# Kernel optimization log

Measured on AMD Instinct MI355X. Metric: run time of the kernel, lower is better.

Reference implementation:

```python
import jax, jax.numpy as jnp
import numpy as np
from jax import lax

Q = 8          # num quantization bins (co_matrix_shape[0])
K = 3          # spatial filter size (spatial_shape = [K,K,K])
PAD = (K - 1) // 2


def setup_inputs() -> dict:
    key = jax.random.key(0)
    k1, k2, k3 = jax.random.split(key, 3)
    # uniform [0,1) so floor((x-min)/max * Q) stays in [0, Q-1] (matches valid torch index_select)
    x = jax.random.uniform(k1, (8, 16, 256, 256), dtype=jnp.float32)
    co_matrix = jax.random.normal(k2, (Q, Q), dtype=jnp.float32)
    spatial_filter = jax.random.normal(k3, (K, K, K), dtype=jnp.float32)
    return {"input": x, "co_matrix": co_matrix, "spatial_filter": spatial_filter}


def _quantize(x, num_q):
    # faithful to the torch code: norm = (x - min) / max  (NOT max-min)
    x_min = jnp.min(x)
    x_max = jnp.max(x)
    idx = jnp.floor((x - x_min) / x_max * num_q).astype(jnp.int32)  # [N,c,h,w]
    return idx


def reference(input, co_matrix, spatial_filter):
    x = input
    N, c, h, w = x.shape
    idx = _quantize(x, Q)                                  # [N,c,h,w] int32

    # Vectorize the per-bin loop: gather row i of co_matrix at every pixel's bin index.
    # cof[i] = co_matrix[i, idx]  -> [Q,N,c,h,w]
    cof = co_matrix[:, idx]
    conv_in = (cof * x[None]).reshape(Q * N, 1, c, h, w)   # [Q*N,1,c,h,w]

    w3d = spatial_filter.reshape(1, 1, K, K, K)
    spatial = lax.conv_general_dilated(
        conv_in, w3d,
        window_strides=(1, 1, 1),
        padding=[(PAD, PAD)] * 3,
        dimension_numbers=("NCDHW", "OIDHW", "NCDHW"),
    ).reshape(Q, N, c, h, w)

    # torch code convolves the mask with a 1x1x1 ones filter at stride 1 -> identity
    mask = (idx[None] == jnp.arange(Q, dtype=jnp.int32)[:, None, None, None, None])
    conv_out = jnp.sum(mask.astype(x.dtype) * spatial, axis=0)  # [N,c,h,w]
    return (conv_out, co_matrix, spatial_filter, idx)
```

## Files before the change

### kernel.cpp

```cpp
#include <hip/hip_runtime.h>
#include <stdint.h>

#define LISTBASE 4096
#define QCAP     4096

__global__ __launch_bounds__(256) void k_minmax(const float* __restrict__ x, int n4, int ntail,
                                                float* __restrict__ partials) {
  __shared__ float smn[256], smx[256];
  int tid = threadIdx.x;
  float mn = 3.0e38f, mx = -3.0e38f;
  const float4* x4 = (const float4*)x;
  for (int i = blockIdx.x * blockDim.x + tid; i < n4; i += gridDim.x * blockDim.x) {
    float4 v = x4[i];
    mn = fminf(mn, fminf(fminf(v.x, v.y), fminf(v.z, v.w)));
    mx = fmaxf(mx, fmaxf(fmaxf(v.x, v.y), fmaxf(v.z, v.w)));
  }
  if (blockIdx.x == 0 && tid == 0) {
    for (int i = 4 * n4; i < 4 * n4 + ntail; ++i) { mn = fminf(mn, x[i]); mx = fmaxf(mx, x[i]); }
  }
  smn[tid] = mn; smx[tid] = mx;
  __syncthreads();
  for (int s = 128; s > 0; s >>= 1) {
    if (tid < s) { smn[tid] = fminf(smn[tid], smn[tid + s]); smx[tid] = fmaxf(smx[tid], smx[tid + s]); }
    __syncthreads();
  }
  if (tid == 0) { partials[2 * blockIdx.x] = smn[0]; partials[2 * blockIdx.x + 1] = smx[0]; }
}

__global__ __launch_bounds__(256) void k_params(const float* __restrict__ partials, int nb,
                                                const float* __restrict__ co, const float* __restrict__ sfil,
                                                float* __restrict__ ws,
                                                float* __restrict__ out_co, float* __restrict__ out_sf) {
  __shared__ float smn[256], smx[256];
  int tid = threadIdx.x;
  float mn = 3.0e38f, mx = -3.0e38f;
  for (int i = tid; i < nb; i += 256) { mn = fminf(mn, partials[2 * i]); mx = fmaxf(mx, partials[2 * i + 1]); }
  smn[tid] = mn; smx[tid] = mx;
  __syncthreads();
  for (int s = 128; s > 0; s >>= 1) {
    if (tid < s) { smn[tid] = fminf(smn[tid], smn[tid + s]); smx[tid] = fmaxf(smx[tid], smx[tid + s]); }
    __syncthreads();
  }
  if (tid == 0) {
    ws[0] = smn[0]; ws[1] = smx[0];
    ws[2] = 1.0f / smx[0];
    ((uint32_t*)ws)[3] = 0u;
  }
  if (tid < 8) {
    const float* r = co + tid * 8;
    float rmn = r[0], rmx = r[0];
    #pragma unroll
    for (int j = 1; j < 8; ++j) { rmn = fminf(rmn, r[j]); rmx = fmaxf(rmx, r[j]); }
    float rs = (rmx - rmn) * (1.0f / 255.0f);
    if (rs < 1e-30f) rs = 1.0f;
    uint32_t d0 = 0, d1 = 0;
    #pragma unroll
    for (int j = 0; j < 8; ++j) {
      int b = (int)lrintf((r[j] - rmn) / rs);
      b = b < 0 ? 0 : (b > 255 ? 255 : b);
      if (j < 4) d0 |= ((uint32_t)b) << (8 * j);
      else       d1 |= ((uint32_t)b) << (8 * (j - 4));
    }
    uint32_t* wsu = (uint32_t*)ws;
    wsu[8 + 4 * tid + 0] = d0;
    wsu[8 + 4 * tid + 1] = d1;
    wsu[8 + 4 * tid + 2] = __float_as_uint(rs);
    wsu[8 + 4 * tid + 3] = __float_as_uint(rmn);
  }
  if (tid < 64) out_co[tid] = co[tid];
  if (tid < 27) out_sf[tid] = sfil[tid];
}

__global__ __launch_bounds__(256) void k_conv(const float* __restrict__ x, const float* __restrict__ sfil,
                                              float* __restrict__ ws, int listcap,
                                              float* __restrict__ out, float* __restrict__ out_idx) {
  __shared__ __align__(16) float    xs[7920];
  __shared__ __align__(16) uint32_t qls[1980];
  __shared__ __align__(16) uint4    tbl[8];

  int tid = threadIdx.x;
  int b = blockIdx.x;
  int wt = b & 1, ht = (b >> 1) & 31, ct = (b >> 6) & 3, n = b >> 8;
  int c0 = ct * 4, h0 = ht * 8, w0 = wt * 128;
  int nbase = n * 16;

  const uint32_t* wsu = (const uint32_t*)ws;
  if (tid < 8) tbl[tid] = ((const uint4*)(wsu + 8))[tid];

  float mn = ws[0], mx = ws[1], y = ws[2];
  uint32_t* cnt = (uint32_t*)ws + 3;
  int* list = (int*)ws + LISTBASE;

  for (int e = tid; e < 1980; e += 256) {
    int lc = e / 330;
    int r  = e - lc * 330;
    int lh = r / 33;
    int lg = r - lh * 33;
    int c = c0 - 1 + lc, h = h0 - 1 + lh, wb = w0 - 1 + 4 * lg;
    bool chok = ((unsigned)c < 16u) & ((unsigned)h < 256u);
    int gofs = ((nbase + c) << 16) + (h << 8) + wb;
    float xv[4]; int qi[4]; uint32_t qu[4];
    #pragma unroll
    for (int j = 0; j < 4; ++j) {
      float xj = 0.0f;
      if (chok & ((unsigned)(wb + j) < 256u)) xj = x[gofs + j];
      float s  = xj - mn;
      float t0 = s * y;
      float r0 = __builtin_fmaf(-mx, t0, s);
      float t1 = __builtin_fmaf(r0, y, t0);
      float r1 = __builtin_fmaf(-mx, t1, s);
      float d  = __builtin_fmaf(r1, y, t1);
      int q = (int)(d * 8.0f);
      xv[j] = xj; qi[j] = q;
      qu[j] = (uint32_t)(q > 7 ? 7 : q);
    }
    if (((qi[0] | qi[1] | qi[2] | qi[3]) & 8) != 0) {
      #pragma unroll
      for (int j = 0; j < 4; ++j) if (qi[j] == 8) {
        uint32_t slot = atomicAdd(cnt, 1u);
        if (slot < (uint32_t)listcap) list[slot] = gofs + j;
      }
    }
    uint32_t b01 = __builtin_amdgcn_perm(qu[1], qu[0], 0x0c0c0400u);
    uint32_t b23 = __builtin_amdgcn_perm(qu[3], qu[2], 0x04000c0cu);
    int ro = lc * 10 + lh;
    *(float4*)&xs[ro * 132 + 4 * lg] = float4{xv[0], xv[1], xv[2], xv[3]};
    qls[ro * 33 + lg] = b01 | b23;
  }
  __syncthreads();

  float wf[27];
  #pragma unroll
  for (int i = 0; i < 27; ++i) wf[i] = sfil[i];

  const int tw = tid & 31, th = tid >> 5;
  const uint32_t SELK[4] = {0x03020100u, 0x04030201u, 0x05040302u, 0x06050403u};

  for (int c = 0; c < 4; ++c) {
    int xbase = (c * 10 + th) * 132 + 4 * tw;
    int qbase = (c * 10 + th) * 33 + tw;

    int qc = qbase + 11 * 33;
    uint32_t Qc0 = qls[qc], Qc1 = qls[qc + 1];
    uint32_t q4 = __builtin_amdgcn_perm(Qc1, Qc0, 0x04030201u);
    uint32_t rlo[4], rhi[4]; float rs4[4], rc4[4];
    #pragma unroll
    for (int k = 0; k < 4; ++k) {
      uint32_t qk = (q4 >> (8 * k)) & 0xffu;
      uint4 T = tbl[qk];
      rlo[k] = T.x; rhi[k] = T.y;
      rs4[k] = __uint_as_float(T.z); rc4[k] = __uint_as_float(T.w);
    }

    float acc1[4] = {0.f, 0.f, 0.f, 0.f};
    float acc2[4] = {0.f, 0.f, 0.f, 0.f};
    #pragma unroll
    for (int dc = 0; dc < 3; ++dc) {
      #pragma unroll
      for (int di = 0; di < 3; ++di) {
        int xo = xbase + (dc * 10 + di) * 132;
        float4 A = *(const float4*)&xs[xo];
        float2 B = *(const float2*)&xs[xo + 4];
        int qo = qbase + (dc * 10 + di) * 33;
        uint32_t Q0 = qls[qo], Q1 = qls[qo + 1];
        float xw[6] = {A.x, A.y, A.z, A.w, B.x, B.y};
        const float* wr = &wf[dc * 9 + di * 3];
        #pragma unroll
        for (int k = 0; k < 4; ++k) {
          uint32_t sel = __builtin_amdgcn_perm(Q1, Q0, SELK[k]);
          uint32_t bb  = __builtin_amdgcn_perm(rhi[k], rlo[k], sel);
          float b0 = (float)(bb & 0xffu);
          float b1 = (float)((bb >> 8) & 0xffu);
          float b2 = (float)((bb >> 16) & 0xffu);
          float p0 = wr[0] * xw[k];
          float p1 = wr[1] * xw[k + 1];
          float p2 = wr[2] * xw[k + 2];
          acc2[k] += p0 + p1 + p2;
          acc1[k] = __builtin_fmaf(p0, b0, acc1[k]);
          acc1[k] = __builtin_fmaf(p1, b1, acc1[k]);
          acc1[k] = __builtin_fmaf(p2, b2, acc1[k]);
        }
      }
    }
    int gbase = ((nbase + c0 + c) << 16) + ((h0 + th) << 8) + (w0 + 4 * tw);
    float4 o;
    o.x = __builtin_fmaf(rs4[0], acc1[0], rc4[0] * acc2[0]);
    o.y = __builtin_fmaf(rs4[1], acc1[1], rc4[1] * acc2[1]);
    o.z = __builtin_fmaf(rs4[2], acc1[2], rc4[2] * acc2[2]);
    o.w = __builtin_fmaf(rs4[3], acc1[3], rc4[3] * acc2[3]);
    *(float4*)&out[gbase] = o;
    out_idx[gbase + 0] = (float)(q4 & 0xffu);
    out_idx[gbase + 1] = (float)((q4 >> 8) & 0xffu);
    out_idx[gbase + 2] = (float)((q4 >> 16) & 0xffu);
    out_idx[gbase + 3] = (float)((q4 >> 24) & 0xffu);
  }
}

__global__ __launch_bounds__(256) void k_fix(const float* __restrict__ ws, int listcap,
                                             float* __restrict__ out, float* __restrict__ out_idx) {
  uint32_t n = ((const uint32_t*)ws)[3];
  if (n > (uint32_t)listcap) n = (uint32_t)listcap;
  const int* list = (const int*)ws + LISTBASE;
  for (uint32_t i = threadIdx.x; i < n; i += 256) {
    int p = list[i];
    out[p] = 0.0f;
    out_idx[p] = 8.0f;
  }
}

extern "C" void kernel_launch(void* const* d_in, const int* in_sizes, int n_in,
                              void* d_out, int out_size, void* d_ws, size_t ws_size,
                              hipStream_t stream) {
  const float* x    = (const float*)d_in[0];
  const float* co   = (const float*)d_in[1];
  const float* sfil = (const float*)d_in[2];
  float* out = (float*)d_out;
  float* ws  = (float*)d_ws;
  int nx = in_sizes[0];

  int nb1 = 1024;
  long wsd = (long)(ws_size / 4);
  long maxnb = (wsd - 64) / 2;
  if (maxnb > 2016) maxnb = 2016;
  if (nb1 > maxnb) nb1 = (int)(maxnb < 1 ? 1 : maxnb);
  int listcap = (int)(wsd - LISTBASE);
  if (listcap > QCAP) listcap = QCAP;
  if (listcap < 0) listcap = 0;

  float* partials = ws + 64;
  int n4 = nx / 4, ntail = nx - 4 * n4;

  float* out_co  = out + nx;
  float* out_sf  = out + nx + 64;
  float* out_idx = out + nx + 64 + 27;

  k_minmax<<<nb1, 256, 0, stream>>>(x, n4, ntail, partials);
  k_params<<<1, 256, 0, stream>>>(partials, nb1, co, sfil, ws, out_co, out_sf);
  k_conv<<<2048, 256, 0, stream>>>(x, sfil, ws, listcap, out, out_idx);
  k_fix<<<1, 256, 0, stream>>>(ws, listcap, out, out_idx);
}
```

Measured before the change: 139.9 us.

## Fuse min/max reduction via atomics, drop fix kernel, halve channel tile

Replaces the two-kernel min/max reduction with a single kernel that publishes its result through order-preserving atomicMin/atomicMax on mapped floats, with the co-matrix table setup folded into block 0. The separate fix-up kernel and its atomic overflow list are removed. The conv kernel now recomputes the exact quantization index for centre pixels, zeroing the output and writing index 8 in place. The conv tile shrinks from 4 channels to 2 and the grid doubles, which cuts shared memory per block at the cost of more halo reloads. Two memset calls are added to initialise the atomic slots.

Measured after the change: 182.5 us. +30.4%, slower.

```diff
diff --git a/kernel.cpp b/kernel.cpp
--- a/kernel.cpp
+++ b/kernel.cpp
@@ -1,11 +1,18 @@
 #include <hip/hip_runtime.h>
 #include <stdint.h>
 
-#define LISTBASE 4096
-#define QCAP     4096
+__device__ __forceinline__ uint32_t mapf(float f) {
+  uint32_t u = __float_as_uint(f);
+  return (u & 0x80000000u) ? ~u : (u | 0x80000000u);
+}
+__device__ __forceinline__ float unmapf(uint32_t m) {
+  return (m & 0x80000000u) ? __uint_as_float(m & 0x7FFFFFFFu) : __uint_as_float(~m);
+}
 
 __global__ __launch_bounds__(256) void k_minmax(const float* __restrict__ x, int n4, int ntail,
-                                                float* __restrict__ partials) {
+                                                const float* __restrict__ co, const float* __restrict__ sfil,
+                                                uint32_t* __restrict__ wsu,
+                                                float* __restrict__ out_co, float* __restrict__ out_sf) {
   __shared__ float smn[256], smx[256];
   int tid = threadIdx.x;
   float mn = 3.0e38f, mx = -3.0e38f;
@@ -24,74 +31,56 @@
     if (tid < s) { smn[tid] = fminf(smn[tid], smn[tid + s]); smx[tid] = fmaxf(smx[tid], smx[tid + s]); }
     __syncthreads();
   }
-  if (tid == 0) { partials[2 * blockIdx.x] = smn[0]; partials[2 * blockIdx.x + 1] = smx[0]; }
-}
-
-__global__ __launch_bounds__(256) void k_params(const float* __restrict__ partials, int nb,
-                                                const float* __restrict__ co, const float* __restrict__ sfil,
-                                                float* __restrict__ ws,
-                                                float* __restrict__ out_co, float* __restrict__ out_sf) {
-  __shared__ float smn[256], smx[256];
-  int tid = threadIdx.x;
-  float mn = 3.0e38f, mx = -3.0e38f;
-  for (int i = tid; i < nb; i += 256) { mn = fminf(mn, partials[2 * i]); mx = fmaxf(mx, partials[2 * i + 1]); }
-  smn[tid] = mn; smx[tid] = mx;
-  __syncthreads();
-  for (int s = 128; s > 0; s >>= 1) {
-    if (tid < s) { smn[tid] = fminf(smn[tid], smn[tid + s]); smx[tid] = fmaxf(smx[tid], smx[tid + s]); }
-    __syncthreads();
-  }
   if (tid == 0) {
-    ws[0] = smn[0]; ws[1] = smx[0];
-    ws[2] = 1.0f / smx[0];
-    ((uint32_t*)ws)[3] = 0u;
-  }
-  if (tid < 8) {
-    const float* r = co + tid * 8;
-    float rmn = r[0], rmx = r[0];
-    #pragma unroll
-    for (int j = 1; j < 8; ++j) { rmn = fminf(rmn, r[j]); rmx = fmaxf(rmx, r[j]); }
-    float rs = (rmx - rmn) * (1.0f / 255.0f);
-    if (rs < 1e-30f) rs = 1.0f;
-    uint32_t d0 = 0, d1 = 0;
-    #pragma unroll
-    for (int j = 0; j < 8; ++j) {
-      int b = (int)lrintf((r[j] - rmn) / rs);
-      b = b < 0 ? 0 : (b > 255 ? 255 : b);
-      if (j < 4) d0 |= ((uint32_t)b) << (8 * j);
-      else       d1 |= ((uint32_t)b) << (8 * (j - 4));
-    }
-    uint32_t* wsu = (uint32_t*)ws;
-    wsu[8 + 4 * tid + 0] = d0;
-    wsu[8 + 4 * tid + 1] = d1;
-    wsu[8 + 4 * tid + 2] = __float_as_uint(rs);
-    wsu[8 + 4 * tid + 3] = __float_as_uint(rmn);
-  }
-  if (tid < 64) out_co[tid] = co[tid];
-  if (tid < 27) out_sf[tid] = sfil[tid];
+    atomicMin(&wsu[0], mapf(smn[0]));
+    atomicMax(&wsu[1], mapf(smx[0]));
+  }
+  if (blockIdx.x == 0) {
+    if (tid < 8) {
+      const float* r = co + tid * 8;
+      float rmn = r[0], rmx = r[0];
+      #pragma unroll
+      for (int j = 1; j < 8; ++j) { rmn = fminf(rmn, r[j]); rmx = fmaxf(rmx, r[j]); }
+      float rs = (rmx - rmn) * (1.0f / 255.0f);
+      if (rs < 1e-30f) rs = 1.0f;
+      uint32_t d0 = 0, d1 = 0;
+      #pragma unroll
+      for (int j = 0; j < 8; ++j) {
+        int b = (int)lrintf((r[j] - rmn) / rs);
+        b = b < 0 ? 0 : (b > 255 ? 255 : b);
+        if (j < 4) d0 |= ((uint32_t)b) << (8 * j);
+        else       d1 |= ((uint32_t)b) << (8 * (j - 4));
+      }
+      wsu[8 + 4 * tid + 0] = d0;
+      wsu[8 + 4 * tid + 1] = d1;
+      wsu[8 + 4 * tid + 2] = __float_as_uint(rs);
+      wsu[8 + 4 * tid + 3] = __float_as_uint(rmn);
+    }
+    if (tid < 64) out_co[tid] = co[tid];
+    if (tid < 27) out_sf[tid] = sfil[tid];
+  }
 }
 
 __global__ __launch_bounds__(256) void k_conv(const float* __restrict__ x, const float* __restrict__ sfil,
-                                              float* __restrict__ ws, int listcap,
+                                              const uint32_t* __restrict__ wsu,
                                               float* __restrict__ out, float* __restrict__ out_idx) {
-  __shared__ __align__(16) float    xs[7920];
-  __shared__ __align__(16) uint32_t qls[1980];
+  __shared__ __align__(16) float    xs[5280];
+  __shared__ __align__(16) uint32_t qls[1320];
   __shared__ __align__(16) uint4    tbl[8];
 
   int tid = threadIdx.x;
   int b = blockIdx.x;
-  int wt = b & 1, ht = (b >> 1) & 31, ct = (b >> 6) & 3, n = b >> 8;
-  int c0 = ct * 4, h0 = ht * 8, w0 = wt * 128;
+  int wt = b & 1, ht = (b >> 1) & 31, ct = (b >> 6) & 7, n = b >> 9;
+  int c0 = ct * 2, h0 = ht * 8, w0 = wt * 128;
   int nbase = n * 16;
 
-  const uint32_t* wsu = (const uint32_t*)ws;
   if (tid < 8) tbl[tid] = ((const uint4*)(wsu + 8))[tid];
 
-  float mn = ws[0], mx = ws[1], y = ws[2];
-  uint32_t* cnt = (uint32_t*)ws + 3;
-  int* list = (int*)ws + LISTBASE;
-
-  for (int e = tid; e < 1980; e += 256) {
+  float mn = unmapf(wsu[0]);
+  float mx = unmapf(wsu[1]);
+  float y  = 1.0f / mx;
+
+  for (int e = tid; e < 1320; e += 256) {
     int lc = e / 330;
     int r  = e - lc * 330;
     int lh = r / 33;
@@ -99,7 +88,7 @@
     int c = c0 - 1 + lc, h = h0 - 1 + lh, wb = w0 - 1 + 4 * lg;
     bool chok = ((unsigned)c < 16u) & ((unsigned)h < 256u);
     int gofs = ((nbase + c) << 16) + (h << 8) + wb;
-    float xv[4]; int qi[4]; uint32_t qu[4];
+    float xv[4]; uint32_t qu[4];
     #pragma unroll
     for (int j = 0; j < 4; ++j) {
       float xj = 0.0f;
@@ -111,15 +100,8 @@
       float r1 = __builtin_fmaf(-mx, t1, s);
       float d  = __builtin_fmaf(r1, y, t1);
       int q = (int)(d * 8.0f);
-      xv[j] = xj; qi[j] = q;
+      xv[j] = xj;
       qu[j] = (uint32_t)(q > 7 ? 7 : q);
-    }
-    if (((qi[0] | qi[1] | qi[2] | qi[3]) & 8) != 0) {
-      #pragma unroll
-      for (int j = 0; j < 4; ++j) if (qi[j] == 8) {
-        uint32_t slot = atomicAdd(cnt, 1u);
-        if (slot < (uint32_t)listcap) list[slot] = gofs + j;
-      }
     }
     uint32_t b01 = __builtin_amdgcn_perm(qu[1], qu[0], 0x0c0c0400u);
     uint32_t b23 = __builtin_amdgcn_perm(qu[3], qu[2], 0x04000c0cu);
@@ -136,7 +118,7 @@
   const int tw = tid & 31, th = tid >> 5;
   const uint32_t SELK[4] = {0x03020100u, 0x04030201u, 0x05040302u, 0x06050403u};
 
-  for (int c = 0; c < 4; ++c) {
+  for (int c = 0; c < 2; ++c) {
     int xbase = (c * 10 + th) * 132 + 4 * tw;
     int qbase = (c * 10 + th) * 33 + tw;
 
@@ -154,6 +136,7 @@
 
     float acc1[4] = {0.f, 0.f, 0.f, 0.f};
     float acc2[4] = {0.f, 0.f, 0.f, 0.f};
+    float4 cxA; float2 cxB;
     #pragma unroll
     for (int dc = 0; dc < 3; ++dc) {
       #pragma unroll
@@ -161,6 +144,7 @@
         int xo = xbase + (dc * 10 + di) * 132;
         float4 A = *(const float4*)&xs[xo];
         float2 B = *(const float2*)&xs[xo + 4];
+        if (dc == 1 && di == 1) { cxA = A; cxB = B; }
         int qo = qbase + (dc * 10 + di) * 33;
         uint32_t Q0 = qls[qo], Q1 = qls[qo + 1];
         float xw[6] = {A.x, A.y, A.z, A.w, B.x, B.y};
@@ -182,29 +166,31 @@
         }
       }
     }
+
+    float cx[4] = {cxA.y, cxA.z, cxA.w, cxB.x};
+    int qt[4];
+    #pragma unroll
+    for (int k = 0; k < 4; ++k) {
+      float s  = cx[k] - mn;
+      float t0 = s * y;
+      float r0 = __builtin_fmaf(-mx, t0, s);
+      float t1 = __builtin_fmaf(r0, y, t0);
+      float r1 = __builtin_fmaf(-mx, t1, s);
+      float d  = __builtin_fmaf(r1, y, t1);
+      qt[k] = (int)(d * 8.0f);
+    }
+
     int gbase = ((nbase + c0 + c) << 16) + ((h0 + th) << 8) + (w0 + 4 * tw);
     float4 o;
-    o.x = __builtin_fmaf(rs4[0], acc1[0], rc4[0] * acc2[0]);
-    o.y = __builtin_fmaf(rs4[1], acc1[1], rc4[1] * acc2[1]);
-    o.z = __builtin_fmaf(rs4[2], acc1[2], rc4[2] * acc2[2]);
-    o.w = __builtin_fmaf(rs4[3], acc1[3], rc4[3] * acc2[3]);
+    o.x = qt[0] > 7 ? 0.0f : __builtin_fmaf(rs4[0], acc1[0], rc4[0] * acc2[0]);
+    o.y = qt[1] > 7 ? 0.0f : __builtin_fmaf(rs4[1], acc1[1], rc4[1] * acc2[1]);
+    o.z = qt[2] > 7 ? 0.0f : __builtin_fmaf(rs4[2], acc1[2], rc4[2] * acc2[2]);
+    o.w = qt[3] > 7 ? 0.0f : __builtin_fmaf(rs4[3], acc1[3], rc4[3] * acc2[3]);
     *(float4*)&out[gbase] = o;
-    out_idx[gbase + 0] = (float)(q4 & 0xffu);
-    out_idx[gbase + 1] = (float)((q4 >> 8) & 0xffu);
-    out_idx[gbase + 2] = (float)((q4 >> 16) & 0xffu);
-    out_idx[gbase + 3] = (float)((q4 >> 24) & 0xffu);
-  }
-}
-
-__global__ __launch_bounds__(256) void k_fix(const float* __restrict__ ws, int listcap,
-                                             float* __restrict__ out, float* __restrict__ out_idx) {
-  uint32_t n = ((const uint32_t*)ws)[3];
-  if (n > (uint32_t)listcap) n = (uint32_t)listcap;
-  const int* list = (const int*)ws + LISTBASE;
-  for (uint32_t i = threadIdx.x; i < n; i += 256) {
-    int p = list[i];
-    out[p] = 0.0f;
-    out_idx[p] = 8.0f;
+    out_idx[gbase + 0] = (float)qt[0];
+    out_idx[gbase + 1] = (float)qt[1];
+    out_idx[gbase + 2] = (float)qt[2];
+    out_idx[gbase + 3] = (float)qt[3];
   }
 }
 
@@ -215,27 +201,18 @@
   const float* co   = (const float*)d_in[1];
   const float* sfil = (const float*)d_in[2];
   float* out = (float*)d_out;
-  float* ws  = (float*)d_ws;
+  uint32_t* wsu = (uint32_t*)d_ws;
   int nx = in_sizes[0];
 
-  int nb1 = 1024;
-  long wsd = (long)(ws_size / 4);
-  long maxnb = (wsd - 64) / 2;
-  if (maxnb > 2016) maxnb = 2016;
-  if (nb1 > maxnb) nb1 = (int)(maxnb < 1 ? 1 : maxnb);
-  int listcap = (int)(wsd - LISTBASE);
-  if (listcap > QCAP) listcap = QCAP;
-  if (listcap < 0) listcap = 0;
-
-  float* partials = ws + 64;
   int n4 = nx / 4, ntail = nx - 4 * n4;
 
   float* out_co  = out + nx;
   float* out_sf  = out + nx + 64;
   float* out_idx = out + nx + 64 + 27;
 
-  k_minmax<<<nb1, 256, 0, stream>>>(x, n4, ntail, partials);
-  k_params<<<1, 256, 0, stream>>>(partials, nb1, co, sfil, ws, out_co, out_sf);
-  k_conv<<<2048, 256, 0, stream>>>(x, sfil, ws, listcap, out, out_idx);
-  k_fix<<<1, 256, 0, stream>>>(ws, listcap, out, out_idx);
-}
+  hipMemsetAsync(wsu + 0, 0xFF, 4, stream);
+  hipMemsetAsync(wsu + 1, 0x00, 4, stream);
+
+  k_minmax<<<2048, 256, 0, stream>>>(x, n4, ntail, co, sfil, wsu, out_co, out_sf);
+  k_conv<<<4096, 256, 0, stream>>>(x, sfil, wsu, out, out_idx);
+}
```
